# Kernel tuning notes

Measured on AMD Instinct MI355X. Metric: run time of the kernel, lower is better.

The kernel has to match this reference:

```python
import jax, jax.numpy as jnp
import numpy as np

B, S, D, O, H = 4, 2048, 1024, 1024, 8


def setup_inputs() -> dict:
    key = jax.random.key(0)
    ks = jax.random.split(key, 5)
    sD = 1.0 / np.sqrt(D)
    x = jax.random.normal(ks[0], (B, S, D), dtype=jnp.float32)
    gate_w = jax.random.uniform(ks[1], (H, D), jnp.float32, -sD, sD)
    gate_b = jax.random.uniform(ks[2], (H,), jnp.float32, -sD, sD)
    expert_w = jax.random.uniform(ks[3], (H, O, D), jnp.float32, -sD, sD)
    expert_b = jax.random.uniform(ks[4], (H, O), jnp.float32, -sD, sD)
    return {"x": x, "gate_w": gate_w, "gate_b": gate_b,
            "expert_w": expert_w, "expert_b": expert_b}


def reference(x, gate_w, gate_b, expert_w, expert_b):
    # gating: [B,S,H], softmax over experts (heads)
    g = jax.nn.softmax(jnp.einsum('bsd,hd->bsh', x, gate_w) + gate_b, axis=-1)
    # fused expert GEMM + weighted accumulation (avoids [B,S,O,H] stack)
    out = jnp.einsum('bsd,hod,bsh->bso', x, expert_w, g)
    out = out + jnp.einsum('bsh,ho->bso', g, expert_b)
    return out
```

## Files before the change

kernel.cpp:

```cpp
#include <hip/hip_runtime.h>
#include <hip/hip_bf16.h>
#include <stdint.h>

#define B_  4
#define S_  2048
#define BS_ (B_ * S_)
#define D_  1024
#define O_  1024
#define H_  8

#define BM 256
#define BN 128
#define BK 64
#define NT 128

typedef unsigned short u16;
typedef __attribute__((ext_vector_type(8))) short     short8;
typedef __attribute__((ext_vector_type(8))) unsigned short ushort8v;
typedef __attribute__((ext_vector_type(4))) float     f32x4;

__device__ __forceinline__ u16 f2bf(float f) {
  unsigned u = __float_as_uint(f);
  unsigned r = (u + 0x7fffu + ((u >> 16) & 1u)) >> 16;
  return (u16)r;
}

#define GLOAD16(gp, lp)                                                        \
  __builtin_amdgcn_global_load_lds(                                            \
      (const __attribute__((address_space(1))) void*)(gp),                     \
      (__attribute__((address_space(3))) void*)(lp), 16, 0, 0)

__global__ __launch_bounds__(256) void gate_conv_kernel(
    const float* __restrict__ x, const float* __restrict__ gate_w,
    const float* __restrict__ gate_b, u16* __restrict__ x_bf,
    float* __restrict__ g_out) {
  const int wave  = threadIdx.x >> 6;
  const int lane  = threadIdx.x & 63;
  const int token = blockIdx.x * 4 + wave;
  const float* xr = x + (size_t)token * D_;
  const int d0 = lane * 16;

  float4 xv[4];
#pragma unroll
  for (int i = 0; i < 4; ++i) xv[i] = *(const float4*)(xr + d0 + i * 4);

  ushort8v lo, hi;
#pragma unroll
  for (int i = 0; i < 2; ++i) {
    lo[i * 4 + 0] = f2bf(xv[i].x); lo[i * 4 + 1] = f2bf(xv[i].y);
    lo[i * 4 + 2] = f2bf(xv[i].z); lo[i * 4 + 3] = f2bf(xv[i].w);
    hi[i * 4 + 0] = f2bf(xv[2 + i].x); hi[i * 4 + 1] = f2bf(xv[2 + i].y);
    hi[i * 4 + 2] = f2bf(xv[2 + i].z); hi[i * 4 + 3] = f2bf(xv[2 + i].w);
  }
  *(ushort8v*)(x_bf + (size_t)token * D_ + d0) = lo;
  *(ushort8v*)(x_bf + (size_t)token * D_ + d0 + 8) = hi;

  float s[H_];
#pragma unroll
  for (int h = 0; h < H_; ++h) {
    const float* gw = gate_w + h * D_ + d0;
    float a = 0.f;
#pragma unroll
    for (int i = 0; i < 4; ++i) {
      float4 w = *(const float4*)(gw + i * 4);
      a += xv[i].x * w.x + xv[i].y * w.y + xv[i].z * w.z + xv[i].w * w.w;
    }
    s[h] = a;
  }
#pragma unroll
  for (int h = 0; h < H_; ++h) {
#pragma unroll
    for (int off = 32; off > 0; off >>= 1) s[h] += __shfl_xor(s[h], off);
    s[h] += gate_b[h];
  }
  float m = s[0];
#pragma unroll
  for (int h = 1; h < H_; ++h) m = fmaxf(m, s[h]);
  float sum = 0.f;
#pragma unroll
  for (int h = 0; h < H_; ++h) { s[h] = expf(s[h] - m); sum += s[h]; }
  const float inv = 1.0f / sum;
#pragma unroll
  for (int h = 0; h < H_; ++h) s[h] *= inv;

  if (lane == 0) {
    float4 g0 = make_float4(s[0], s[1], s[2], s[3]);
    float4 g1 = make_float4(s[4], s[5], s[6], s[7]);
    *(float4*)(g_out + (size_t)token * H_)     = g0;
    *(float4*)(g_out + (size_t)token * H_ + 4) = g1;
  }
}

__global__ __launch_bounds__(256) void convw_kernel(
    const float* __restrict__ w, u16* __restrict__ wb) {
  size_t i = ((size_t)blockIdx.x * 256 + threadIdx.x) * 8;
  float4 a = *(const float4*)(w + i);
  float4 b = *(const float4*)(w + i + 4);
  ushort8v v;
  v[0] = f2bf(a.x); v[1] = f2bf(a.y); v[2] = f2bf(a.z); v[3] = f2bf(a.w);
  v[4] = f2bf(b.x); v[5] = f2bf(b.y); v[6] = f2bf(b.z); v[7] = f2bf(b.w);
  *(ushort8v*)(wb + i) = v;
}

__global__ __launch_bounds__(512, 2) void moe_gemm_kernel(
    const u16* __restrict__ Xb, const u16* __restrict__ Wb,
    const float* __restrict__ g, const float* __restrict__ eb,
    float* __restrict__ out) {
  __shared__ __align__(16) u16 As[3][BM * BK];
  __shared__ __align__(16) u16 Bs[3][BN * BK];
  __shared__ float gs[H_][BM];
  __shared__ float ebs[H_][BN];

  const int tid  = threadIdx.x;
  const int wave = tid >> 6;
  const int lane = tid & 63;

  const int bx   = blockIdx.x;
  const int row0 = ((bx & 7) * 4 + (bx >> 6)) * BM;
  const int col0 = ((bx >> 3) & 7) * BN;

  for (int i = tid; i < H_ * BM; i += 512) {
    int h = i >> 8, r = i & 255;
    gs[h][r] = g[(size_t)(row0 + r) * H_ + h];
  }
  for (int i = tid; i < H_ * BN; i += 512) {
    int h = i >> 7, c = i & 127;
    ebs[h][c] = eb[h * O_ + col0 + c];
  }

  const int wm = wave >> 1;
  const int wn = wave & 1;

  const int s_row = wave * 8 + (lane >> 3);
  const int s_col = ((lane & 7) * 8) ^ (((lane >> 3) & 7) << 3);
  const u16* a_base = Xb + (size_t)(row0 + s_row) * D_ + s_col;
  const u16* b_base = Wb + (size_t)(col0 + s_row) * D_ + s_col;
  const int lds_off = (wave * 8) * BK;

  const int sw  = (lane & 7) << 3;
  const int aq  = lane >> 4;
  const int ce0 = (aq * 8) ^ sw;
  const int ce1 = (aq * 8 + 32) ^ sw;
  const int arow = (wm * 64 + (lane & 15)) * BK;
  const int brow = (wn * 64 + (lane & 15)) * BK;

  const f32x4 zero4 = {0.f, 0.f, 0.f, 0.f};
  f32x4 acc[4][4], part[4][4];
#pragma unroll
  for (int i = 0; i < 4; ++i)
#pragma unroll
    for (int j = 0; j < 4; ++j) { acc[i][j] = zero4; part[i][j] = zero4; }

#pragma unroll
  for (int i = 0; i < 4; ++i)
    GLOAD16(a_base + (size_t)(i * 64) * D_, &As[0][lds_off + i * 64 * BK]);
#pragma unroll
  for (int j = 0; j < 2; ++j)
    GLOAD16(b_base + (size_t)(j * 64) * D_, &Bs[0][lds_off + j * 64 * BK]);
#pragma unroll
  for (int i = 0; i < 4; ++i)
    GLOAD16(a_base + (size_t)(i * 64) * D_ + 64, &As[1][lds_off + i * 64 * BK]);
#pragma unroll
  for (int j = 0; j < 2; ++j)
    GLOAD16(b_base + (size_t)(j * 64) * D_ + 64, &Bs[1][lds_off + j * 64 * BK]);

  asm volatile("s_waitcnt vmcnt(6) lgkmcnt(0)" ::: "memory");
  __builtin_amdgcn_s_barrier();

  int buf = 0;
  for (int t = 0; t < NT; ++t) {
    const u16* Ab = &As[buf][0];
    const u16* Bb = &Bs[buf][0];
    const int t2 = t + 2;
    const int sbuf = (buf + 2 >= 3) ? buf - 1 : buf + 2;

    short8 af0[4], bf0[4], af1[4], bf1[4];
#pragma unroll
    for (int fm = 0; fm < 4; ++fm)
      af0[fm] = *(const short8*)&Ab[arow + fm * 16 * BK + ce0];
#pragma unroll
    for (int fn = 0; fn < 4; ++fn)
      bf0[fn] = *(const short8*)&Bb[brow + fn * 16 * BK + ce0];
#pragma unroll
    for (int fm = 0; fm < 4; ++fm)
      af1[fm] = *(const short8*)&Ab[arow + fm * 16 * BK + ce1];
#pragma unroll
    for (int fn = 0; fn < 4; ++fn)
      bf1[fn] = *(const short8*)&Bb[brow + fn * 16 * BK + ce1];

    if (t2 < NT) {
      const size_t koff = (size_t)((t2 & 15) * 64);
#pragma unroll
      for (int i = 0; i < 4; ++i)
        GLOAD16(a_base + (size_t)(i * 64) * D_ + koff,
                &As[sbuf][lds_off + i * 64 * BK]);
      const size_t boff = ((size_t)(t2 >> 4) * O_) * D_ + koff;
#pragma unroll
      for (int j = 0; j < 2; ++j)
        GLOAD16(b_base + (size_t)(j * 64) * D_ + boff,
                &Bs[sbuf][lds_off + j * 64 * BK]);
    }

    __builtin_amdgcn_s_setprio(1);
#pragma unroll
    for (int fm = 0; fm < 4; ++fm)
#pragma unroll
      for (int fn = 0; fn < 4; ++fn)
        part[fm][fn] = __builtin_amdgcn_mfma_f32_16x16x32_bf16(
            af0[fm], bf0[fn], part[fm][fn], 0, 0, 0);
#pragma unroll
    for (int fm = 0; fm < 4; ++fm)
#pragma unroll
      for (int fn = 0; fn < 4; ++fn)
        part[fm][fn] = __builtin_amdgcn_mfma_f32_16x16x32_bf16(
            af1[fm], bf1[fn], part[fm][fn], 0, 0, 0);
    __builtin_amdgcn_s_setprio(0);

    if (t < NT - 2) {
      asm volatile("s_waitcnt vmcnt(6)" ::: "memory");
    } else {
      asm volatile("s_waitcnt vmcnt(0)" ::: "memory");
    }
    __builtin_amdgcn_s_barrier();

    if ((t & 15) == 15) {
      const int h = t >> 4;
      float ebv[4];
#pragma unroll
      for (int fn = 0; fn < 4; ++fn)
        ebv[fn] = ebs[h][wn * 64 + fn * 16 + (lane & 15)];
#pragma unroll
      for (int fm = 0; fm < 4; ++fm) {
        const f32x4 gg =
            *(const f32x4*)&gs[h][wm * 64 + fm * 16 + (lane >> 4) * 4];
#pragma unroll
        for (int fn = 0; fn < 4; ++fn)
#pragma unroll
          for (int j = 0; j < 4; ++j) {
            acc[fm][fn][j] += gg[j] * (part[fm][fn][j] + ebv[fn]);
            part[fm][fn][j] = 0.f;
          }
      }
    }

    buf = (buf == 2) ? 0 : buf + 1;
  }

  const int crow = row0 + wm * 64 + (lane >> 4) * 4;
  const int ccol = col0 + wn * 64 + (lane & 15);
#pragma unroll
  for (int fm = 0; fm < 4; ++fm)
#pragma unroll
    for (int fn = 0; fn < 4; ++fn)
#pragma unroll
      for (int j = 0; j < 4; ++j)
        out[(size_t)(crow + fm * 16 + j) * O_ + (ccol + fn * 16)] =
            acc[fm][fn][j];
}

extern "C" void kernel_launch(void* const* d_in, const int* in_sizes, int n_in,
                              void* d_out, int out_size, void* d_ws,
                              size_t ws_size, hipStream_t stream) {
  const float* x   = (const float*)d_in[0];
  const float* gw  = (const float*)d_in[1];
  const float* gb  = (const float*)d_in[2];
  const float* ew  = (const float*)d_in[3];
  const float* ebp = (const float*)d_in[4];
  float* out = (float*)d_out;

  u16*   x_bf = (u16*)d_ws;
  u16*   w_bf = (u16*)((char*)d_ws + (size_t)BS_ * D_ * 2);
  float* gbuf = (float*)((char*)d_ws + (size_t)BS_ * D_ * 2 +
                         (size_t)H_ * O_ * D_ * 2);

  gate_conv_kernel<<<BS_ / 4, 256, 0, stream>>>(x, gw, gb, x_bf, gbuf);
  convw_kernel<<<(H_ * O_ * D_) / 2048, 256, 0, stream>>>(ew, w_bf);
  moe_gemm_kernel<<<(BS_ / BM) * (O_ / BN), 512, 0, stream>>>(x_bf, w_bf, gbuf,
                                                              ebp, out);
}
```

Before: 158.3 us.

## Shrink GEMM tile to 128x128 with 256 threads and double buffering

Halves the M tile from 256 to 128 rows and runs the block with 4 waves instead of 8. The LDS pipeline drops from triple to double buffering and now waits on vmcnt(0) every iteration. The gate-weight load is rewritten as a per-row loop. This doubles the grid to 512 blocks for better CU coverage, at the cost of less data reuse per block and less latency hiding in the prefetch pipeline.

```diff
diff --git a/kernel.cpp b/kernel.cpp
--- a/kernel.cpp
+++ b/kernel.cpp
@@ -9,7 +9,7 @@
 #define O_  1024
 #define H_  8
 
-#define BM 256
+#define BM 128
 #define BN 128
 #define BK 64
 #define NT 128
@@ -102,12 +102,12 @@
   *(ushort8v*)(wb + i) = v;
 }
 
-__global__ __launch_bounds__(512, 2) void moe_gemm_kernel(
+__global__ __launch_bounds__(256) void moe_gemm_kernel(
     const u16* __restrict__ Xb, const u16* __restrict__ Wb,
     const float* __restrict__ g, const float* __restrict__ eb,
     float* __restrict__ out) {
-  __shared__ __align__(16) u16 As[3][BM * BK];
-  __shared__ __align__(16) u16 Bs[3][BN * BK];
+  __shared__ __align__(16) u16 As[2][BM * BK];
+  __shared__ __align__(16) u16 Bs[2][BN * BK];
   __shared__ float gs[H_][BM];
   __shared__ float ebs[H_][BN];
 
@@ -116,14 +116,15 @@
   const int lane = tid & 63;
 
   const int bx   = blockIdx.x;
-  const int row0 = ((bx & 7) * 4 + (bx >> 6)) * BM;
+  const int row0 = ((bx & 7) * 8 + (bx >> 6)) * BM;
   const int col0 = ((bx >> 3) & 7) * BN;
 
-  for (int i = tid; i < H_ * BM; i += 512) {
-    int h = i >> 8, r = i & 255;
-    gs[h][r] = g[(size_t)(row0 + r) * H_ + h];
-  }
-  for (int i = tid; i < H_ * BN; i += 512) {
+  if (tid < BM) {
+    const float* gr = g + (size_t)(row0 + tid) * H_;
+#pragma unroll
+    for (int h = 0; h < H_; ++h) gs[h][tid] = gr[h];
+  }
+  for (int i = tid; i < H_ * BN; i += 256) {
     int h = i >> 7, c = i & 127;
     ebs[h][c] = eb[h * O_ + col0 + c];
   }
@@ -136,6 +137,23 @@
   const u16* a_base = Xb + (size_t)(row0 + s_row) * D_ + s_col;
   const u16* b_base = Wb + (size_t)(col0 + s_row) * D_ + s_col;
   const int lds_off = (wave * 8) * BK;
+
+#define STAGE_A(kk_, buf_)                                                     \
+  {                                                                            \
+    const u16* ap = a_base + (size_t)(kk_) * BK;                               \
+    GLOAD16(ap,                     &As[buf_][lds_off]);                       \
+    GLOAD16(ap + (size_t)32  * D_,  &As[buf_][lds_off + 32 * BK]);             \
+    GLOAD16(ap + (size_t)64  * D_,  &As[buf_][lds_off + 64 * BK]);             \
+    GLOAD16(ap + (size_t)96  * D_,  &As[buf_][lds_off + 96 * BK]);             \
+  }
+#define STAGE_B(off_, buf_)                                                    \
+  {                                                                            \
+    const u16* bp = b_base + (off_);                                           \
+    GLOAD16(bp,                     &Bs[buf_][lds_off]);                       \
+    GLOAD16(bp + (size_t)32  * D_,  &Bs[buf_][lds_off + 32 * BK]);             \
+    GLOAD16(bp + (size_t)64  * D_,  &Bs[buf_][lds_off + 64 * BK]);             \
+    GLOAD16(bp + (size_t)96  * D_,  &Bs[buf_][lds_off + 96 * BK]);             \
+  }
 
   const int sw  = (lane & 7) << 3;
   const int aq  = lane >> 4;
@@ -151,28 +169,14 @@
 #pragma unroll
     for (int j = 0; j < 4; ++j) { acc[i][j] = zero4; part[i][j] = zero4; }
 
-#pragma unroll
-  for (int i = 0; i < 4; ++i)
-    GLOAD16(a_base + (size_t)(i * 64) * D_, &As[0][lds_off + i * 64 * BK]);
-#pragma unroll
-  for (int j = 0; j < 2; ++j)
-    GLOAD16(b_base + (size_t)(j * 64) * D_, &Bs[0][lds_off + j * 64 * BK]);
-#pragma unroll
-  for (int i = 0; i < 4; ++i)
-    GLOAD16(a_base + (size_t)(i * 64) * D_ + 64, &As[1][lds_off + i * 64 * BK]);
-#pragma unroll
-  for (int j = 0; j < 2; ++j)
-    GLOAD16(b_base + (size_t)(j * 64) * D_ + 64, &Bs[1][lds_off + j * 64 * BK]);
-
-  asm volatile("s_waitcnt vmcnt(6) lgkmcnt(0)" ::: "memory");
+  STAGE_A(0, 0);
+  STAGE_B(0, 0);
+  asm volatile("s_waitcnt vmcnt(0) lgkmcnt(0)" ::: "memory");
   __builtin_amdgcn_s_barrier();
 
-  int buf = 0;
   for (int t = 0; t < NT; ++t) {
-    const u16* Ab = &As[buf][0];
-    const u16* Bb = &Bs[buf][0];
-    const int t2 = t + 2;
-    const int sbuf = (buf + 2 >= 3) ? buf - 1 : buf + 2;
+    const u16* Ab = &As[t & 1][0];
+    const u16* Bb = &Bs[t & 1][0];
 
     short8 af0[4], bf0[4], af1[4], bf1[4];
 #pragma unroll
@@ -188,17 +192,11 @@
     for (int fn = 0; fn < 4; ++fn)
       bf1[fn] = *(const short8*)&Bb[brow + fn * 16 * BK + ce1];
 
-    if (t2 < NT) {
-      const size_t koff = (size_t)((t2 & 15) * 64);
-#pragma unroll
-      for (int i = 0; i < 4; ++i)
-        GLOAD16(a_base + (size_t)(i * 64) * D_ + koff,
-                &As[sbuf][lds_off + i * 64 * BK]);
-      const size_t boff = ((size_t)(t2 >> 4) * O_) * D_ + koff;
-#pragma unroll
-      for (int j = 0; j < 2; ++j)
-        GLOAD16(b_base + (size_t)(j * 64) * D_ + boff,
-                &Bs[sbuf][lds_off + j * 64 * BK]);
+    if (t + 1 < NT) {
+      const int t1 = t + 1;
+      STAGE_A((t1 & 15), (t1 & 1));
+      STAGE_B(((size_t)(t1 >> 4) * O_) * D_ + (size_t)((t1 & 15) * 64),
+              (t1 & 1));
     }
 
     __builtin_amdgcn_s_setprio(1);
@@ -216,11 +214,7 @@
             af1[fm], bf1[fn], part[fm][fn], 0, 0, 0);
     __builtin_amdgcn_s_setprio(0);
 
-    if (t < NT - 2) {
-      asm volatile("s_waitcnt vmcnt(6)" ::: "memory");
-    } else {
-      asm volatile("s_waitcnt vmcnt(0)" ::: "memory");
-    }
+    asm volatile("s_waitcnt vmcnt(0)" ::: "memory");
     __builtin_amdgcn_s_barrier();
 
     if ((t & 15) == 15) {
@@ -242,8 +236,6 @@
           }
       }
     }
-
-    buf = (buf == 2) ? 0 : buf + 1;
   }
 
   const int crow = row0 + wm * 64 + (lane >> 4) * 4;
@@ -275,6 +267,6 @@
 
   gate_conv_kernel<<<BS_ / 4, 256, 0, stream>>>(x, gw, gb, x_bf, gbuf);
   convw_kernel<<<(H_ * O_ * D_) / 2048, 256, 0, stream>>>(ew, w_bf);
-  moe_gemm_kernel<<<(BS_ / BM) * (O_ / BN), 512, 0, stream>>>(x_bf, w_bf, gbuf,
+  moe_gemm_kernel<<<(BS_ / BM) * (O_ / BN), 256, 0, stream>>>(x_bf, w_bf, gbuf,
                                                               ebp, out);
 }
```

New measurement: 228.6 us. 44.4% more time.
